# Performance work log

Hardware: AMD Instinct MI355X
Metric: run time of the kernel (lower is better)

Reference implementation:

```python
import jax, jax.numpy as jnp
import numpy as np

B, N, C, D, T = 8, 2048, 16, 64, 32
H = 100  # msg-MLP hidden width


def setup_inputs() -> dict:
    key = jax.random.key(0)
    ks = jax.random.split(key, 24)
    s = 0.05
    rn = lambda k, shape: (jax.random.normal(k, shape) * s).astype(jnp.float32)
    inp = {
        "Mvv": jax.random.bernoulli(ks[0], 0.05, (B, N, N)).astype(jnp.float32),
        "ch_init": jax.random.uniform(ks[1], (B, C, D), jnp.float32),
        "v_init": (jax.random.normal(ks[2], (D,)) / jnp.sqrt(jnp.float32(D))).astype(jnp.float32),
        # vertex LSTMCell: input 2D -> hidden D (gate order i,f,g,o as in torch)
        "v_Wih": rn(ks[3], (4 * D, 2 * D)), "v_Whh": rn(ks[4], (4 * D, D)),
        "v_bih": rn(ks[5], (4 * D,)), "v_bhh": rn(ks[6], (4 * D,)),
        # color LSTMCell: input D -> hidden D
        "c_Wih": rn(ks[7], (4 * D, D)), "c_Whh": rn(ks[8], (4 * D, D)),
        "c_bih": rn(ks[9], (4 * D,)), "c_bhh": rn(ks[10], (4 * D,)),
        # c_msg_mlp: D->100->D with ReLU after each Linear
        "cmsg_W1": rn(ks[11], (H, D)), "cmsg_b1": rn(ks[12], (H,)),
        "cmsg_W2": rn(ks[13], (D, H)), "cmsg_b2": rn(ks[14], (D,)),
        # v_msg_mlp: D->100->D
        "vmsg_W1": rn(ks[15], (H, D)), "vmsg_b1": rn(ks[16], (H,)),
        "vmsg_W2": rn(ks[17], (D, H)), "vmsg_b2": rn(ks[18], (D,)),
        # vote MLP: D -> D//4 -> 1 with Sigmoid in between
        "vote_W1": rn(ks[19], (D // 4, D)), "vote_b1": rn(ks[20], (D // 4,)),
        "vote_W2": rn(ks[21], (1, D // 4)), "vote_b2": rn(ks[22], (1,)),
        "n_colors": jax.random.randint(ks[23], (B,), 1, C + 1),
    }
    return inp


def _lstm_cell(x, h, c, Wih, Whh, bih, bhh):
    g = x @ Wih.T + bih + h @ Whh.T + bhh
    i, f, gg, o = jnp.split(g, 4, axis=-1)
    c2 = jax.nn.sigmoid(f) * c + jax.nn.sigmoid(i) * jnp.tanh(gg)
    h2 = jax.nn.sigmoid(o) * jnp.tanh(c2)
    return h2, c2


def _msg_mlp(x, W1, b1, W2, b2):
    return jax.nn.relu(jax.nn.relu(x @ W1.T + b1) @ W2.T + b2)


def reference(Mvv, ch_init, v_init,
              v_Wih, v_Whh, v_bih, v_bhh,
              c_Wih, c_Whh, c_bih, c_bhh,
              cmsg_W1, cmsg_b1, cmsg_W2, cmsg_b2,
              vmsg_W1, vmsg_b1, vmsg_W2, vmsg_b2,
              vote_W1, vote_b1, vote_W2, vote_b2,
              n_colors):
    A = Mvv + jnp.eye(N, dtype=Mvv.dtype)[None]                 # [B,N,N] self-loops
    col_mask = (jnp.arange(C)[None, :] < n_colors[:, None])     # [B,C]
    Mvc = jnp.broadcast_to(col_mask[:, None, :], (B, N, C)).astype(Mvv.dtype)  # [B,N,C]

    vh0 = jnp.broadcast_to(v_init, (B, N, D)).astype(Mvv.dtype)
    state0 = (vh0, jnp.zeros((B, N, D), Mvv.dtype), ch_init, jnp.zeros((B, C, D), Mvv.dtype))

    def step(st, _):
        vh, vc, ch, cc = st
        c_msg = _msg_mlp(ch, cmsg_W1, cmsg_b1, cmsg_W2, cmsg_b2)          # [B,C,D]
        v_in = jnp.concatenate([A @ vh, Mvc @ c_msg], axis=-1)            # [B,N,2D]
        vh, vc = _lstm_cell(v_in, vh, vc, v_Wih, v_Whh, v_bih, v_bhh)
        v_msg = _msg_mlp(vh, vmsg_W1, vmsg_b1, vmsg_W2, vmsg_b2)          # [B,N,D]
        c_in = jnp.einsum('bnc,bnd->bcd', Mvc, v_msg)                     # [B,C,D]
        ch, cc = _lstm_cell(c_in, ch, cc, c_Wih, c_Whh, c_bih, c_bhh)
        return (vh, vc, ch, cc), None

    (vh, _, _, _), _ = jax.lax.scan(step, state0, None, length=T)

    # dropout is identity in eval mode
    vote = jax.nn.sigmoid(vh @ vote_W1.T + vote_b1) @ vote_W2.T + vote_b2  # [B,N,1]
    pred = jax.nn.sigmoid(jnp.mean(vote, axis=1)).squeeze(-1)              # [B]
    return pred


if __name__ == "__main__":
    out = reference(**setup_inputs())
    print(out.shape, out)
```

## Files before the change

### kernel.cpp

```cpp
#include <hip/hip_runtime.h>

#define Bk 8
#define Nk 2048
#define Ck 16
#define Dk 64
#define Tk 32
#define GBLK 256
#define NTHR 512
#define SLOT (Bk * 64 * 2048)

typedef __attribute__((ext_vector_type(8))) short short8;
typedef __attribute__((ext_vector_type(4))) float floatx4;
typedef __attribute__((ext_vector_type(4))) unsigned uint4v;
typedef unsigned long long u64;
typedef unsigned short u16;

#define OFF_WCAT 0
#define OFF_VW1  69632
#define OFF_AT   85760
#define OFF_HT   103168
#define OFF_HROW 120576
#define OFF_CH   129792
#define OFF_CC   133888
#define OFF_GC   137984
#define OFF_VBS  139008
#define OFF_CBS  140032
#define OFF_VB1  141056
#define OFF_VB2  141568
#define OFF_CB1  141824
#define OFF_CB2  142336
#define OFF_W1V  142592
#define OFF_B1V  146688
#define OFF_W2V  146752
#define OFF_VAC  146816
#define OFF_VMS  147072
#define OFF_CMS  147328
#define OFF_VOT  147584
#define LDS_TOTAL 149632

__device__ __forceinline__ float b2f(u16 u) {
  return __uint_as_float(((unsigned)u) << 16);
}
__device__ __forceinline__ u16 f2b(float f) {
  unsigned u = __float_as_uint(f);
  unsigned r = (u + 0x7FFFu + ((u >> 16) & 1u)) >> 16;
  return (u16)r;
}
__device__ __forceinline__ float sigf(float x) { return 1.0f / (1.0f + __expf(-x)); }
__device__ __forceinline__ float tanhf_(float x) { return 2.0f / (1.0f + __expf(-2.0f * x)) - 1.0f; }

__device__ __forceinline__ void ld_sys_b128(uint4v& dst, const void* p) {
  asm volatile("global_load_dwordx4 %0, %1, off sc0 sc1" : "=v"(dst) : "v"(p) : "memory");
}
__device__ __forceinline__ void ld_b128(uint4v& dst, const void* p) {
  asm volatile("global_load_dwordx4 %0, %1, off" : "=v"(dst) : "v"(p) : "memory");
}
__device__ __forceinline__ void st_sys_b128(void* p, uint4v v) {
  asm volatile("global_store_dwordx4 %0, %1, off sc0 sc1" :: "v"(p), "v"(v) : "memory");
}
#define WAITVM(n) asm volatile("s_waitcnt vmcnt(" #n ")" ::: "memory")
__device__ __forceinline__ void barrier_lgkm() {
  asm volatile("s_waitcnt lgkmcnt(0)\n\ts_barrier" ::: "memory");
}

__device__ __forceinline__ void s_agent_f32(float* p, float v) {
  __hip_atomic_store(p, v, __ATOMIC_RELAXED, __HIP_MEMORY_SCOPE_AGENT);
}
__device__ __forceinline__ float l_agent_f32(const float* p) {
  return __hip_atomic_load(p, __ATOMIC_RELAXED, __HIP_MEMORY_SCOPE_AGENT);
}

__global__ void k_init_w(const float* vWih, const float* vWhh, const float* cWih, const float* cWhh,
                         const float* vm1, const float* vm2, const float* cm1, const float* cm2,
                         u16* wcat, u16* cwcat, u16* vw1, u16* vw2, u16* cw1, u16* cw2,
                         unsigned* bar, float* voteAcc, u64* diagBits) {
  const int tid = threadIdx.x;
  for (int i = tid; i < 256 * 128; i += 256) {
    int g = i >> 7, k = i & 127;
    wcat[i]  = f2b(k < 64 ? vWih[g * 128 + k] : vWhh[g * 64 + (k - 64)]);
    cwcat[i] = f2b(k < 64 ? cWih[g * 64 + k]  : cWhh[g * 64 + (k - 64)]);
  }
  for (int i = tid; i < 112 * 64; i += 256) {
    int j = i >> 6, k = i & 63;
    vw1[i] = f2b(j < 100 ? vm1[j * 64 + k] : 0.f);
    cw1[i] = f2b(j < 100 ? cm1[j * 64 + k] : 0.f);
  }
  for (int i = tid; i < 64 * 128; i += 256) {
    int d = i >> 7, k = i & 127;
    vw2[i] = f2b(k < 100 ? vm2[d * 100 + k] : 0.f);
    cw2[i] = f2b(k < 100 ? cm2[d * 100 + k] : 0.f);
  }
  for (int i = tid; i < 1024; i += 256) bar[i] = 0u;
  if (tid < 8) voteAcc[tid] = 0.f;
  if (tid < 256) diagBits[tid] = 0ull;
}

__global__ void k_init_vt(const float* vInit, u16* vt0) {
  for (int i = blockIdx.x * blockDim.x + threadIdx.x; i < SLOT; i += gridDim.x * blockDim.x) {
    int d = (i >> 11) & 63;
    vt0[i] = f2b(vInit[d]);
  }
}

__global__ void k_bits(const float* Mvv, u64* Abits, u64* diagBits) {
  const int lane = threadIdx.x & 63;
  const int wid = blockIdx.x * 4 + (threadIdx.x >> 6);
  const int b = wid >> 11, n = wid & 2047;
  const float* row = Mvv + (size_t)wid * Nk;
  u64* dst = Abits + (size_t)wid * 32;
  for (int w64 = 0; w64 < 32; ++w64) {
    float v = row[w64 * 64 + lane];
    u64 m = __ballot(v != 0.0f);
    if (lane == 0) {
      if (w64 == (n >> 6)) {
        if ((m >> (n & 63)) & 1ull)
          atomicOr(diagBits + b * 32 + (n >> 6), 1ull << (n & 63));
        m |= 1ull << (n & 63);
      }
      dst[w64] = m;
    }
  }
}

struct PArgs {
  const float *vWih, *chInit;
  const float *vbih, *vbhh, *cbih, *cbhh;
  const float *vmb1, *vmb2, *cmb1, *cmb2;
  const float *voW1, *vob1, *voW2, *vob2;
  const int* ncolors;
  u16* vhbuf;
  const u64* Abits;
  const u64* diagBits;
  float* partial;
  const u16 *wcat, *cwcat, *vw1, *vw2, *cw1, *cw2;
  unsigned* bar;
  float* voteAcc;
  float* out;
};

__device__ __forceinline__ void gridbar(unsigned* bar, unsigned target) {
  WAITVM(0);
  __syncthreads();
  if (threadIdx.x == 0) {
    atomicAdd(bar, 1u);
    int guard = 0;
    while (__hip_atomic_load(bar, __ATOMIC_RELAXED, __HIP_MEMORY_SCOPE_AGENT) < target) {
      __builtin_amdgcn_s_sleep(2);
      if (++guard > (1 << 24)) break;
    }
  }
  __syncthreads();
}

__global__ void __launch_bounds__(NTHR, 1) k_persist(PArgs A) {
  extern __shared__ char smem[];
  u16* WcatU  = (u16*)(smem + OFF_WCAT);
  u16* vW1U   = (u16*)(smem + OFF_VW1);
  u16* AtileU = (u16*)(smem + OFF_AT);
  u16* HtileU = (u16*)(smem + OFF_HT);
  u16* HrowU  = (u16*)(smem + OFF_HROW);
  float* chl = (float*)(smem + OFF_CH);
  float* ccl = (float*)(smem + OFF_CC);
  float* gc  = (float*)(smem + OFF_GC);
  float* vbs = (float*)(smem + OFF_VBS);
  float* cbs = (float*)(smem + OFF_CBS);
  float* vb1 = (float*)(smem + OFF_VB1);
  float* vb2 = (float*)(smem + OFF_VB2);
  float* cb1 = (float*)(smem + OFF_CB1);
  float* cb2 = (float*)(smem + OFF_CB2);
  float* W1v = (float*)(smem + OFF_W1V);
  float* b1v = (float*)(smem + OFF_B1V);
  float* W2v = (float*)(smem + OFF_W2V);
  float* vac = (float*)(smem + OFF_VAC);
  float* vms = (float*)(smem + OFF_VMS);
  float* cms = (float*)(smem + OFF_CMS);
  float* vot = (float*)(smem + OFF_VOT);

  const int tid = threadIdx.x;
  const int lane = tid & 63;
  const int w = tid >> 6;
  const int rt = w & 3;
  const int gh = w >> 2;
  const int q = lane >> 4;
  const int l15 = lane & 15;
  const int bb = blockIdx.x & 7;
  const int rb = (blockIdx.x >> 3) * 64;
  const int ncolv = A.ncolors[bb];
  const floatx4 zf = {0.f, 0.f, 0.f, 0.f};
  unsigned* mybar = A.bar + bb * 64;

  for (int i = tid; i < 256 * 128; i += NTHR) { int g = i >> 7, k = i & 127; WcatU[g * 136 + k] = A.wcat[i]; }
  for (int i = tid; i < 112 * 64; i += NTHR)  { int j = i >> 6, k = i & 63;  vW1U[j * 72 + k]  = A.vw1[i]; }
  if (tid < 112) { vb1[tid] = (tid < 100) ? A.vmb1[tid] : 0.f; cb1[tid] = (tid < 100) ? A.cmb1[tid] : 0.f; }
  if (tid < 64)  { vb2[tid] = A.vmb2[tid]; cb2[tid] = A.cmb2[tid]; vac[tid] = 0.f; }
  if (tid < 256) { vbs[tid] = A.vbih[tid] + A.vbhh[tid]; cbs[tid] = A.cbih[tid] + A.cbhh[tid]; }
  for (int i = tid; i < 1024; i += NTHR) { W1v[i] = A.voW1[i]; chl[i] = A.chInit[bb * 1024 + i]; ccl[i] = 0.f; }
  if (tid < 16) { b1v[tid] = A.vob1[tid]; W2v[tid] = A.voW2[tid]; }
  const u64 diagbits = A.diagBits[bb * 32 + (rb >> 6)];
  __syncthreads();

  auto cmsgPhase = [&]() {
    for (int i = tid; i < 1024; i += NTHR) { int c = i >> 6, kk = i & 63; AtileU[c * 136 + kk] = f2b(chl[i]); }
    __syncthreads();
    if (w < 7) {
      floatx4 m1a = zf;
#pragma unroll
      for (int ks = 0; ks < 2; ++ks) {
        short8 af = *(const short8*)(AtileU + l15 * 136 + ks * 32 + q * 8);
        short8 b0 = *(const short8*)(A.cw1 + (size_t)((w * 16 + l15) * 64 + ks * 32 + q * 8));
        m1a = __builtin_amdgcn_mfma_f32_16x16x32_bf16(af, b0, m1a, 0, 0, 0);
      }
#pragma unroll
      for (int reg = 0; reg < 4; ++reg) {
        float hv = m1a[reg] + cb1[w * 16 + l15];
        HtileU[(q * 4 + reg) * 136 + w * 16 + l15] = f2b(hv > 0.f ? hv : 0.f);
      }
    }
    if (tid < 128) {
      int r = tid >> 3, c = 112 + (tid & 7) * 2;
      HtileU[r * 136 + c] = 0; HtileU[r * 136 + c + 1] = 0;
    }
    __syncthreads();
    if (w < 4) {
      floatx4 m2 = zf;
#pragma unroll
      for (int ks = 0; ks < 4; ++ks) {
        short8 af = *(const short8*)(HtileU + l15 * 136 + ks * 32 + q * 8);
        short8 bv = *(const short8*)(A.cw2 + (size_t)((w * 16 + l15) * 128 + ks * 32 + q * 8));
        m2 = __builtin_amdgcn_mfma_f32_16x16x32_bf16(af, bv, m2, 0, 0, 0);
      }
      float s2 = 0.f;
#pragma unroll
      for (int reg = 0; reg < 4; ++reg) {
        int c = q * 4 + reg;
        float v = m2[reg] + cb2[w * 16 + l15];
        v = v > 0.f ? v : 0.f;
        if (c < ncolv) s2 += v;
      }
      s2 += __shfl_xor(s2, 16);
      s2 += __shfl_xor(s2, 32);
      if (q == 0) cms[w * 16 + l15] = s2;
    }
    __syncthreads();
    if (tid < 256) {
      float dot = 0.f;
      const float* wr = A.vWih + tid * 128 + 64;
#pragma unroll
      for (int k2 = 0; k2 < 64; ++k2) dot += cms[k2] * wr[k2];
      gc[tid] = dot + vbs[tid];
    }
    __syncthreads();
  };

  float vc[4][4] = {};
  u16 hreg[16];
  if (!gh) {
    u16 h0 = A.vhbuf[(size_t)(bb * 64 + lane) * 2048 + rb];
#pragma unroll
    for (int r = 0; r < 16; ++r) hreg[r] = h0;
  }

  cmsgPhase();
  unsigned ep = 0;

  const u64* arow = A.Abits + ((size_t)bb * 2048 + rb + rt * 16 + l15) * 32;

  for (int t = 0; t < Tk; ++t) {
    const u16* vtr = A.vhbuf + (size_t)(t & 1) * SLOT + (size_t)bb * 64 * 2048;
    u16* vtw = A.vhbuf + (size_t)((t & 1) ^ 1) * SLOT + (size_t)bb * 64 * 2048;

    floatx4 acc4[4];
#pragma unroll
    for (int nt = 0; nt < 4; ++nt) acc4[nt] = zf;

    uint4v D[2][2];
    uint4v Bts[4];

    auto issueGroup = [&](int c, uint4v (&Ds)[2], uint4v& Bv) {
      ld_b128(Bv, (const char*)arow + (size_t)c * 16);
      const char* base = (const char*)vtr + (size_t)c * 256;
#pragma unroll
      for (int i = 0; i < 2; ++i) {
        int idx = i * NTHR + tid, d = idx >> 4, j2 = idx & 15;
        ld_sys_b128(Ds[i], base + (size_t)d * 4096 + j2 * 16);
      }
    };
    auto stageGroup = [&](const uint4v (&Ds)[2], u16* buf) {
#pragma unroll
      for (int i = 0; i < 2; ++i) {
        int idx = i * NTHR + tid, d = idx >> 4, j2 = idx & 15;
        *(uint4v*)((char*)buf + (size_t)d * 272 + j2 * 16) = Ds[i];
      }
    };
    auto mfmaChunk = [&](const u16* buf, u64 w0, u64 w1) {
      u64 wsel = gh ? w1 : w0;
#pragma unroll
      for (int ks = 0; ks < 2; ++ks) {
        unsigned byte = (unsigned)(wsel >> (ks * 32 + q * 8)) & 0xFFu;
        short8 af;
#pragma unroll
        for (int j = 0; j < 8; ++j) af[j] = (short)(((byte >> j) & 1u) ? 0x3F80 : 0);
        int kg = gh * 2 + ks;
#pragma unroll
        for (int nt = 0; nt < 4; ++nt) {
          short8 bv = *(const short8*)(buf + (nt * 16 + l15) * 136 + kg * 32 + q * 8);
          acc4[nt] = __builtin_amdgcn_mfma_f32_16x16x32_bf16(af, bv, acc4[nt], 0, 0, 0);
        }
      }
    };

    issueGroup(0, D[0], Bts[0]);
    issueGroup(1, D[1], Bts[1]);
    WAITVM(3);
    stageGroup(D[0], AtileU);
    issueGroup(2, D[0], Bts[2]);
    barrier_lgkm();

#pragma unroll
    for (int c = 0; c < 16; ++c) {
      if (c < 14) { WAITVM(3); } else { WAITVM(0); }
      if (c < 15) {
        stageGroup(D[(c + 1) & 1], ((c + 1) & 1) ? HtileU : AtileU);
        if (c + 3 < 16) issueGroup(c + 3, D[(c + 1) & 1], Bts[(c + 3) & 3]);
      }
      {
        const uint4v& Bv = Bts[c & 3];
        u64 w0 = ((u64)Bv[1] << 32) | Bv[0];
        u64 w1 = ((u64)Bv[3] << 32) | Bv[2];
        mfmaChunk((c & 1) ? HtileU : AtileU, w0, w1);
      }
      if (c < 15) barrier_lgkm();
    }
    __syncthreads();

    {
      float* ptf = (float*)(smem + OFF_HT);
      if (gh) {
#pragma unroll
        for (int nt = 0; nt < 4; ++nt)
#pragma unroll
          for (int reg = 0; reg < 4; ++reg)
            ptf[rt * 1024 + (nt * 4 + reg) * 64 + lane] = acc4[nt][reg];
      }
      __syncthreads();
      if (!gh) {
#pragma unroll
        for (int nt = 0; nt < 4; ++nt)
#pragma unroll
          for (int reg = 0; reg < 4; ++reg)
            acc4[nt][reg] += ptf[rt * 1024 + (nt * 4 + reg) * 64 + lane];
#pragma unroll
        for (int r = 0; r < 16; ++r) AtileU[(rt * 16 + r) * 136 + 64 + lane] = hreg[r];
#pragma unroll
        for (int nt = 0; nt < 4; ++nt) {
#pragma unroll
          for (int reg = 0; reg < 4; ++reg) {
            int m = rt * 16 + q * 4 + reg;
            float fl = (float)((diagbits >> m) & 1ull);
            float hp = b2f(AtileU[m * 136 + 64 + nt * 16 + l15]);
            AtileU[m * 136 + nt * 16 + l15] = f2b(acc4[nt][reg] + fl * hp);
          }
        }
      }
    }
    __syncthreads();

    floatx4 acc2[8];
#pragma unroll
    for (int j = 0; j < 8; ++j) acc2[j] = zf;
#pragma unroll
    for (int ks = 0; ks < 4; ++ks) {
      short8 af = *(const short8*)(AtileU + (rt * 16 + l15) * 136 + ks * 32 + q * 8);
#pragma unroll
      for (int j = 0; j < 8; ++j) {
        short8 bv = *(const short8*)(WcatU + ((gh * 8 + j) * 16 + l15) * 136 + ks * 32 + q * 8);
        acc2[j] = __builtin_amdgcn_mfma_f32_16x16x32_bf16(af, bv, acc2[j], 0, 0, 0);
      }
    }
    __syncthreads();
    {
      float* gex = (float*)(smem + OFF_AT);
      if (gh) {
#pragma unroll
        for (int j = 0; j < 8; ++j)
#pragma unroll
          for (int reg = 0; reg < 4; ++reg)
            gex[(rt * 16 + q * 4 + reg) * 132 + j * 16 + l15] = acc2[j][reg];
      }
      __syncthreads();
      if (!gh) {
#pragma unroll
        for (int u = 0; u < 4; ++u) {
          const int d2 = u * 16 + l15;
          const float gi = gc[d2], gf2 = gc[64 + d2], gg = gc[128 + d2], go = gc[192 + d2];
#pragma unroll
          for (int reg = 0; reg < 4; ++reg) {
            const int row = rt * 16 + q * 4 + reg;
            float iv = acc2[u][reg] + gi;
            float fv = acc2[u + 4][reg] + gf2;
            float gv = gex[row * 132 + u * 16 + l15] + gg;
            float ov = gex[row * 132 + 64 + u * 16 + l15] + go;
            float cn = sigf(fv) * vc[u][reg] + sigf(iv) * tanhf_(gv);
            vc[u][reg] = cn;
            HrowU[row * 72 + d2] = f2b(sigf(ov) * tanhf_(cn));
          }
        }
      }
    }
    __syncthreads();
    if (!gh) {
#pragma unroll
      for (int r = 0; r < 16; ++r) hreg[r] = HrowU[(rt * 16 + r) * 72 + lane];
    }

    if (gh) {
      if (t < Tk - 1) {
        int lt = tid & 255, d = lt >> 2, rr = (lt & 3) * 16;
        union { u16 s[8]; uint4v v; } p0, p1;
#pragma unroll
        for (int j = 0; j < 8; ++j) {
          p0.s[j] = HrowU[(rr + j) * 72 + d];
          p1.s[j] = HrowU[(rr + 8 + j) * 72 + d];
        }
        char* dst = (char*)(vtw + (size_t)d * 2048 + rb + rr);
        st_sys_b128(dst, p0.v);
        st_sys_b128(dst + 16, p1.v);
      }
    } else if (t < Tk - 1) {
      u16* HID = AtileU;
      floatx4 h1[7];
#pragma unroll
      for (int nt = 0; nt < 7; ++nt) h1[nt] = zf;
#pragma unroll
      for (int ks = 0; ks < 2; ++ks) {
        short8 af = *(const short8*)(HrowU + (rt * 16 + l15) * 72 + ks * 32 + q * 8);
#pragma unroll
        for (int nt = 0; nt < 7; ++nt) {
          short8 bv = *(const short8*)(vW1U + (nt * 16 + l15) * 72 + ks * 32 + q * 8);
          h1[nt] = __builtin_amdgcn_mfma_f32_16x16x32_bf16(af, bv, h1[nt], 0, 0, 0);
        }
      }
#pragma unroll
      for (int nt = 0; nt < 7; ++nt) {
        float bb1 = vb1[nt * 16 + l15];
#pragma unroll
        for (int reg = 0; reg < 4; ++reg) {
          float hv = h1[nt][reg] + bb1;
          HID[(rt * 16 + q * 4 + reg) * 136 + nt * 16 + l15] = f2b(hv > 0.f ? hv : 0.f);
        }
      }
#pragma unroll
      for (int r = 0; r < 4; ++r) HID[(rt * 16 + q * 4 + r) * 136 + 112 + l15] = 0;

      floatx4 vm[4];
#pragma unroll
      for (int nt = 0; nt < 4; ++nt) vm[nt] = zf;
#pragma unroll
      for (int ks = 0; ks < 4; ++ks) {
        short8 af = *(const short8*)(HID + (rt * 16 + l15) * 136 + ks * 32 + q * 8);
#pragma unroll
        for (int nt = 0; nt < 4; ++nt) {
          short8 bv = *(const short8*)(A.vw2 + (size_t)((nt * 16 + l15) * 128 + ks * 32 + q * 8));
          vm[nt] = __builtin_amdgcn_mfma_f32_16x16x32_bf16(af, bv, vm[nt], 0, 0, 0);
        }
      }
#pragma unroll
      for (int u = 0; u < 4; ++u) {
        float bb2 = vb2[u * 16 + l15];
        float s = 0.f;
#pragma unroll
        for (int reg = 0; reg < 4; ++reg) { float v = vm[u][reg] + bb2; s += (v > 0.f ? v : 0.f); }
        s += __shfl_xor(s, 16);
        s += __shfl_xor(s, 32);
        if (q == 0) atomicAdd(&vac[u * 16 + l15], s);
      }
    }

    if (t < Tk - 1) {
      __syncthreads();
      if (tid < 64) {
        s_agent_f32(&A.partial[(size_t)((t & 1) * GBLK + blockIdx.x) * 64 + tid], vac[tid]);
        vac[tid] = 0.f;
      }
      gridbar(mybar, (++ep) * 32);

      if (tid < 64) {
        float s = 0.f;
        const float* pp = A.partial + (size_t)((t & 1) * GBLK) * 64;
        for (int i2 = 0; i2 < 32; ++i2) s += l_agent_f32(&pp[(i2 * 8 + bb) * 64 + tid]);
        vms[tid] = s;
      }
      __syncthreads();
      for (int i2 = tid; i2 < 16 * 128; i2 += NTHR) {
        int c = i2 >> 7, kk = i2 & 127;
        float v = (kk < 64) ? ((c < ncolv) ? vms[kk] : 0.f) : chl[c * 64 + (kk - 64)];
        AtileU[c * 136 + kk] = f2b(v);
      }
      __syncthreads();
      floatx4 cacc[2];
      cacc[0] = zf; cacc[1] = zf;
#pragma unroll
      for (int ks = 0; ks < 4; ++ks) {
        short8 af = *(const short8*)(AtileU + l15 * 136 + ks * 32 + q * 8);
#pragma unroll
        for (int j = 0; j < 2; ++j) {
          short8 bv = *(const short8*)(A.cwcat + (size_t)(((w * 2 + j) * 16 + l15) * 128 + ks * 32 + q * 8));
          cacc[j] = __builtin_amdgcn_mfma_f32_16x16x32_bf16(af, bv, cacc[j], 0, 0, 0);
        }
      }
      __syncthreads();
      float* cgp = (float*)(smem + OFF_AT);
#pragma unroll
      for (int j = 0; j < 2; ++j)
#pragma unroll
        for (int reg = 0; reg < 4; ++reg)
          cgp[(q * 4 + reg) * 260 + (w * 2 + j) * 16 + l15] = cacc[j][reg];
      __syncthreads();
      for (int i2 = tid; i2 < 1024; i2 += NTHR) {
        int c = i2 >> 6, d2 = i2 & 63;
        float iv = cgp[c * 260 + d2] + cbs[d2];
        float fv = cgp[c * 260 + 64 + d2] + cbs[64 + d2];
        float gv = cgp[c * 260 + 128 + d2] + cbs[128 + d2];
        float ov = cgp[c * 260 + 192 + d2] + cbs[192 + d2];
        float cn = sigf(fv) * ccl[i2] + sigf(iv) * tanhf_(gv);
        ccl[i2] = cn;
        chl[i2] = sigf(ov) * tanhf_(cn);
      }
      __syncthreads();
      cmsgPhase();
    }
  }

  {
    int r = tid >> 3, p = tid & 7;
    float hj[2] = {0.f, 0.f};
    for (int d2 = 0; d2 < 64; ++d2) {
      float hv = b2f(HrowU[r * 72 + d2]);
      hj[0] += hv * W1v[(p * 2) * 64 + d2];
      hj[1] += hv * W1v[(p * 2 + 1) * 64 + d2];
    }
    float pv = sigf(hj[0] + b1v[p * 2]) * W2v[p * 2] + sigf(hj[1] + b1v[p * 2 + 1]) * W2v[p * 2 + 1];
    vot[tid] = pv;
  }
  __syncthreads();
  if (tid < 64) {
    float vr = A.vob2[0];
#pragma unroll
    for (int k = 0; k < 8; ++k) vr += vot[tid * 8 + k];
    vr += __shfl_xor(vr, 1);
    vr += __shfl_xor(vr, 2);
    vr += __shfl_xor(vr, 4);
    vr += __shfl_xor(vr, 8);
    vr += __shfl_xor(vr, 16);
    vr += __shfl_xor(vr, 32);
    if (tid == 0) atomicAdd(&A.voteAcc[bb], vr);
  }
  gridbar(mybar, (++ep) * 32);
  if (blockIdx.x < 8 && tid == 0) {
    float m = l_agent_f32(&A.voteAcc[blockIdx.x]) * (1.f / 2048.f);
    A.out[blockIdx.x] = 1.f / (1.f + __expf(-m));
  }
}

extern "C" void kernel_launch(void* const* d_in, const int* in_sizes, int n_in,
                              void* d_out, int out_size, void* d_ws, size_t ws_size,
                              hipStream_t stream) {
  (void)in_sizes; (void)n_in; (void)out_size; (void)ws_size;
  const float* Mvv    = (const float*)d_in[0];
  const float* chInit = (const float*)d_in[1];
  const float* vInit  = (const float*)d_in[2];
  const float* vWih   = (const float*)d_in[3];
  const float* vWhh   = (const float*)d_in[4];
  const float* vbih   = (const float*)d_in[5];
  const float* vbhh   = (const float*)d_in[6];
  const float* cWih   = (const float*)d_in[7];
  const float* cWhh   = (const float*)d_in[8];
  const float* cbih   = (const float*)d_in[9];
  const float* cbhh   = (const float*)d_in[10];
  const float* cm1    = (const float*)d_in[11];
  const float* cmb1   = (const float*)d_in[12];
  const float* cm2    = (const float*)d_in[13];
  const float* cmb2   = (const float*)d_in[14];
  const float* vm1    = (const float*)d_in[15];
  const float* vmb1   = (const float*)d_in[16];
  const float* vm2    = (const float*)d_in[17];
  const float* vmb2   = (const float*)d_in[18];
  const float* voW1   = (const float*)d_in[19];
  const float* vob1   = (const float*)d_in[20];
  const float* voW2   = (const float*)d_in[21];
  const float* vob2   = (const float*)d_in[22];
  const int*   ncol   = (const int*)d_in[23];

  char* wsb = (char*)d_ws;
  size_t off = 0;
  auto wsAlloc = [&](size_t bytes) -> char* {
    char* p = wsb + off;
    off = (off + bytes + 255) & ~(size_t)255;
    return p;
  };
  unsigned* bar   = (unsigned*)wsAlloc(4096);
  float* voteAcc  = (float*)wsAlloc(256);
  u16* vhb        = (u16*)wsAlloc((size_t)2 * SLOT * 2);
  u64* Abits      = (u64*)wsAlloc((size_t)Bk * Nk * 32 * 8);
  u64* diagBits   = (u64*)wsAlloc((size_t)Bk * 32 * 8);
  float* partial  = (float*)wsAlloc((size_t)2 * GBLK * 64 * 4);
  u16* wcat       = (u16*)wsAlloc(256 * 128 * 2);
  u16* cwcat      = (u16*)wsAlloc(256 * 128 * 2);
  u16* vw1        = (u16*)wsAlloc(112 * 64 * 2);
  u16* vw2        = (u16*)wsAlloc(64 * 128 * 2);
  u16* cw1        = (u16*)wsAlloc(112 * 64 * 2);
  u16* cw2        = (u16*)wsAlloc(64 * 128 * 2);

  k_init_w<<<1, 256, 0, stream>>>(vWih, vWhh, cWih, cWhh, vm1, vm2, cm1, cm2,
                                  wcat, cwcat, vw1, vw2, cw1, cw2, bar, voteAcc, diagBits);
  k_init_vt<<<256, 256, 0, stream>>>(vInit, vhb);
  k_bits<<<Bk * Nk / 4, 256, 0, stream>>>(Mvv, Abits, diagBits);

  (void)hipFuncSetAttribute((const void*)k_persist,
                            hipFuncAttributeMaxDynamicSharedMemorySize, LDS_TOTAL);
  PArgs pa;
  pa.vWih = vWih; pa.chInit = chInit;
  pa.vbih = vbih; pa.vbhh = vbhh; pa.cbih = cbih; pa.cbhh = cbhh;
  pa.vmb1 = vmb1; pa.vmb2 = vmb2; pa.cmb1 = cmb1; pa.cmb2 = cmb2;
  pa.voW1 = voW1; pa.vob1 = vob1; pa.voW2 = voW2; pa.vob2 = vob2;
  pa.ncolors = ncol;
  pa.vhbuf = vhb; pa.Abits = Abits; pa.diagBits = diagBits; pa.partial = partial;
  pa.wcat = wcat; pa.cwcat = cwcat; pa.vw1 = vw1; pa.vw2 = vw2; pa.cw1 = cw1; pa.cw2 = cw2;
  pa.bar = bar; pa.voteAcc = voteAcc; pa.out = (float*)d_out;
  k_persist<<<GBLK, NTHR, LDS_TOTAL, stream>>>(pa);
}
```

Measured before the change: 1.497 ms.

## Replace persistent kernel grid barriers with per-timestep kernel launches

Replaces the persistent kernel, which used software grid barriers across blocks, with one kernel launch per timestep plus a final reduction kernel. Cross-step state (vertex cell state, color hidden/cell state, partial sums) moves to global buffers, and loads and stores become ordinary cached accesses instead of system-coherent ones. This removes the spin-wait barrier and the coherence overhead. In exchange it adds 32 launches, reloads all weights into LDS every step, and recomputes the small color LSTM redundantly in every block.

```diff
diff --git a/kernel.cpp b/kernel.cpp
--- a/kernel.cpp
+++ b/kernel.cpp
@@ -21,7 +21,6 @@
 #define OFF_HT   103168
 #define OFF_HROW 120576
 #define OFF_CH   129792
-#define OFF_CC   133888
 #define OFF_GC   137984
 #define OFF_VBS  139008
 #define OFF_CBS  140032
@@ -49,31 +48,18 @@
 __device__ __forceinline__ float sigf(float x) { return 1.0f / (1.0f + __expf(-x)); }
 __device__ __forceinline__ float tanhf_(float x) { return 2.0f / (1.0f + __expf(-2.0f * x)) - 1.0f; }
 
-__device__ __forceinline__ void ld_sys_b128(uint4v& dst, const void* p) {
-  asm volatile("global_load_dwordx4 %0, %1, off sc0 sc1" : "=v"(dst) : "v"(p) : "memory");
-}
 __device__ __forceinline__ void ld_b128(uint4v& dst, const void* p) {
   asm volatile("global_load_dwordx4 %0, %1, off" : "=v"(dst) : "v"(p) : "memory");
-}
-__device__ __forceinline__ void st_sys_b128(void* p, uint4v v) {
-  asm volatile("global_store_dwordx4 %0, %1, off sc0 sc1" :: "v"(p), "v"(v) : "memory");
 }
 #define WAITVM(n) asm volatile("s_waitcnt vmcnt(" #n ")" ::: "memory")
 __device__ __forceinline__ void barrier_lgkm() {
   asm volatile("s_waitcnt lgkmcnt(0)\n\ts_barrier" ::: "memory");
 }
 
-__device__ __forceinline__ void s_agent_f32(float* p, float v) {
-  __hip_atomic_store(p, v, __ATOMIC_RELAXED, __HIP_MEMORY_SCOPE_AGENT);
-}
-__device__ __forceinline__ float l_agent_f32(const float* p) {
-  return __hip_atomic_load(p, __ATOMIC_RELAXED, __HIP_MEMORY_SCOPE_AGENT);
-}
-
 __global__ void k_init_w(const float* vWih, const float* vWhh, const float* cWih, const float* cWhh,
                          const float* vm1, const float* vm2, const float* cm1, const float* cm2,
                          u16* wcat, u16* cwcat, u16* vw1, u16* vw2, u16* cw1, u16* cw2,
-                         unsigned* bar, float* voteAcc, u64* diagBits) {
+                         float* voteAcc, u64* diagBits) {
   const int tid = threadIdx.x;
   for (int i = tid; i < 256 * 128; i += 256) {
     int g = i >> 7, k = i & 127;
@@ -90,7 +76,6 @@
     vw2[i] = f2b(k < 100 ? vm2[d * 100 + k] : 0.f);
     cw2[i] = f2b(k < 100 ? cm2[d * 100 + k] : 0.f);
   }
-  for (int i = tid; i < 1024; i += 256) bar[i] = 0u;
   if (tid < 8) voteAcc[tid] = 0.f;
   if (tid < 256) diagBits[tid] = 0ull;
 }
@@ -122,8 +107,8 @@
   }
 }
 
-struct PArgs {
-  const float *vWih, *chInit;
+struct SArgs {
+  const float *chInit, *vWih;
   const float *vbih, *vbhh, *cbih, *cbhh;
   const float *vmb1, *vmb2, *cmb1, *cmb2;
   const float *voW1, *vob1, *voW2, *vob2;
@@ -132,27 +117,15 @@
   const u64* Abits;
   const u64* diagBits;
   float* partial;
+  float* vcbuf;
+  float* chbuf;
+  float* ccbuf;
   const u16 *wcat, *cwcat, *vw1, *vw2, *cw1, *cw2;
-  unsigned* bar;
   float* voteAcc;
-  float* out;
+  int t;
 };
 
-__device__ __forceinline__ void gridbar(unsigned* bar, unsigned target) {
-  WAITVM(0);
-  __syncthreads();
-  if (threadIdx.x == 0) {
-    atomicAdd(bar, 1u);
-    int guard = 0;
-    while (__hip_atomic_load(bar, __ATOMIC_RELAXED, __HIP_MEMORY_SCOPE_AGENT) < target) {
-      __builtin_amdgcn_s_sleep(2);
-      if (++guard > (1 << 24)) break;
-    }
-  }
-  __syncthreads();
-}
-
-__global__ void __launch_bounds__(NTHR, 1) k_persist(PArgs A) {
+__global__ void __launch_bounds__(NTHR, 1) k_step(SArgs A) {
   extern __shared__ char smem[];
   u16* WcatU  = (u16*)(smem + OFF_WCAT);
   u16* vW1U   = (u16*)(smem + OFF_VW1);
@@ -160,7 +133,6 @@
   u16* HtileU = (u16*)(smem + OFF_HT);
   u16* HrowU  = (u16*)(smem + OFF_HROW);
   float* chl = (float*)(smem + OFF_CH);
-  float* ccl = (float*)(smem + OFF_CC);
   float* gc  = (float*)(smem + OFF_GC);
   float* vbs = (float*)(smem + OFF_VBS);
   float* cbs = (float*)(smem + OFF_CBS);
@@ -176,6 +148,7 @@
   float* cms = (float*)(smem + OFF_CMS);
   float* vot = (float*)(smem + OFF_VOT);
 
+  const int t = A.t;
   const int tid = threadIdx.x;
   const int lane = tid & 63;
   const int w = tid >> 6;
@@ -187,246 +160,291 @@
   const int rb = (blockIdx.x >> 3) * 64;
   const int ncolv = A.ncolors[bb];
   const floatx4 zf = {0.f, 0.f, 0.f, 0.f};
-  unsigned* mybar = A.bar + bb * 64;
 
   for (int i = tid; i < 256 * 128; i += NTHR) { int g = i >> 7, k = i & 127; WcatU[g * 136 + k] = A.wcat[i]; }
   for (int i = tid; i < 112 * 64; i += NTHR)  { int j = i >> 6, k = i & 63;  vW1U[j * 72 + k]  = A.vw1[i]; }
   if (tid < 112) { vb1[tid] = (tid < 100) ? A.vmb1[tid] : 0.f; cb1[tid] = (tid < 100) ? A.cmb1[tid] : 0.f; }
   if (tid < 64)  { vb2[tid] = A.vmb2[tid]; cb2[tid] = A.cmb2[tid]; vac[tid] = 0.f; }
   if (tid < 256) { vbs[tid] = A.vbih[tid] + A.vbhh[tid]; cbs[tid] = A.cbih[tid] + A.cbhh[tid]; }
-  for (int i = tid; i < 1024; i += NTHR) { W1v[i] = A.voW1[i]; chl[i] = A.chInit[bb * 1024 + i]; ccl[i] = 0.f; }
+  for (int i = tid; i < 1024; i += NTHR) W1v[i] = A.voW1[i];
   if (tid < 16) { b1v[tid] = A.vob1[tid]; W2v[tid] = A.voW2[tid]; }
   const u64 diagbits = A.diagBits[bb * 32 + (rb >> 6)];
-  __syncthreads();
-
-  auto cmsgPhase = [&]() {
-    for (int i = tid; i < 1024; i += NTHR) { int c = i >> 6, kk = i & 63; AtileU[c * 136 + kk] = f2b(chl[i]); }
-    __syncthreads();
-    if (w < 7) {
-      floatx4 m1a = zf;
-#pragma unroll
-      for (int ks = 0; ks < 2; ++ks) {
-        short8 af = *(const short8*)(AtileU + l15 * 136 + ks * 32 + q * 8);
-        short8 b0 = *(const short8*)(A.cw1 + (size_t)((w * 16 + l15) * 64 + ks * 32 + q * 8));
-        m1a = __builtin_amdgcn_mfma_f32_16x16x32_bf16(af, b0, m1a, 0, 0, 0);
-      }
-#pragma unroll
-      for (int reg = 0; reg < 4; ++reg) {
-        float hv = m1a[reg] + cb1[w * 16 + l15];
-        HtileU[(q * 4 + reg) * 136 + w * 16 + l15] = f2b(hv > 0.f ? hv : 0.f);
-      }
-    }
-    if (tid < 128) {
-      int r = tid >> 3, c = 112 + (tid & 7) * 2;
-      HtileU[r * 136 + c] = 0; HtileU[r * 136 + c + 1] = 0;
-    }
-    __syncthreads();
-    if (w < 4) {
-      floatx4 m2 = zf;
-#pragma unroll
-      for (int ks = 0; ks < 4; ++ks) {
-        short8 af = *(const short8*)(HtileU + l15 * 136 + ks * 32 + q * 8);
-        short8 bv = *(const short8*)(A.cw2 + (size_t)((w * 16 + l15) * 128 + ks * 32 + q * 8));
-        m2 = __builtin_amdgcn_mfma_f32_16x16x32_bf16(af, bv, m2, 0, 0, 0);
-      }
-      float s2 = 0.f;
-#pragma unroll
-      for (int reg = 0; reg < 4; ++reg) {
-        int c = q * 4 + reg;
-        float v = m2[reg] + cb2[w * 16 + l15];
-        v = v > 0.f ? v : 0.f;
-        if (c < ncolv) s2 += v;
-      }
-      s2 += __shfl_xor(s2, 16);
-      s2 += __shfl_xor(s2, 32);
-      if (q == 0) cms[w * 16 + l15] = s2;
-    }
-    __syncthreads();
-    if (tid < 256) {
-      float dot = 0.f;
-      const float* wr = A.vWih + tid * 128 + 64;
-#pragma unroll
-      for (int k2 = 0; k2 < 64; ++k2) dot += cms[k2] * wr[k2];
-      gc[tid] = dot + vbs[tid];
-    }
-    __syncthreads();
-  };
-
-  float vc[4][4] = {};
+
   u16 hreg[16];
   if (!gh) {
-    u16 h0 = A.vhbuf[(size_t)(bb * 64 + lane) * 2048 + rb];
-#pragma unroll
-    for (int r = 0; r < 16; ++r) hreg[r] = h0;
-  }
-
-  cmsgPhase();
-  unsigned ep = 0;
-
+    const u16* hp = A.vhbuf + (size_t)(t & 1) * SLOT + ((size_t)(bb * 64 + lane)) * 2048 + rb + rt * 16;
+#pragma unroll
+    for (int r = 0; r < 16; ++r) hreg[r] = hp[r];
+  }
+  __syncthreads();
+
+  if (t == 0) {
+    for (int i = tid; i < 1024; i += NTHR) chl[i] = A.chInit[bb * 1024 + i];
+    __syncthreads();
+  } else {
+    const float* chprev = (t == 1) ? (A.chInit + bb * 1024)
+                                   : (A.chbuf + (size_t)((t & 1) ^ 1) * Bk * 1024 + bb * 1024);
+    if (tid < 64) {
+      float s = 0.f;
+      const float* pp = A.partial + (size_t)(((t - 1) & 1) * GBLK) * 64;
+      for (int i2 = 0; i2 < 32; ++i2) s += pp[(i2 * 8 + bb) * 64 + tid];
+      vms[tid] = s;
+    }
+    __syncthreads();
+    for (int i2 = tid; i2 < 16 * 128; i2 += NTHR) {
+      int c = i2 >> 7, kk = i2 & 127;
+      float v = (kk < 64) ? ((c < ncolv) ? vms[kk] : 0.f) : chprev[c * 64 + (kk - 64)];
+      AtileU[c * 136 + kk] = f2b(v);
+    }
+    __syncthreads();
+    floatx4 cacc[2];
+    cacc[0] = zf; cacc[1] = zf;
+#pragma unroll
+    for (int ks = 0; ks < 4; ++ks) {
+      short8 af = *(const short8*)(AtileU + l15 * 136 + ks * 32 + q * 8);
+#pragma unroll
+      for (int j = 0; j < 2; ++j) {
+        short8 bv = *(const short8*)(A.cwcat + (size_t)(((w * 2 + j) * 16 + l15) * 128 + ks * 32 + q * 8));
+        cacc[j] = __builtin_amdgcn_mfma_f32_16x16x32_bf16(af, bv, cacc[j], 0, 0, 0);
+      }
+    }
+    __syncthreads();
+    float* cgp = (float*)(smem + OFF_AT);
+#pragma unroll
+    for (int j = 0; j < 2; ++j)
+#pragma unroll
+      for (int reg = 0; reg < 4; ++reg)
+        cgp[(q * 4 + reg) * 260 + (w * 2 + j) * 16 + l15] = cacc[j][reg];
+    __syncthreads();
+    for (int i2 = tid; i2 < 1024; i2 += NTHR) {
+      int c = i2 >> 6, d2 = i2 & 63;
+      float iv = cgp[c * 260 + d2] + cbs[d2];
+      float fv = cgp[c * 260 + 64 + d2] + cbs[64 + d2];
+      float gv = cgp[c * 260 + 128 + d2] + cbs[128 + d2];
+      float ov = cgp[c * 260 + 192 + d2] + cbs[192 + d2];
+      float ccv = (t == 1) ? 0.f : A.ccbuf[(size_t)((t & 1) ^ 1) * Bk * 1024 + bb * 1024 + i2];
+      float cn = sigf(fv) * ccv + sigf(iv) * tanhf_(gv);
+      float hn = sigf(ov) * tanhf_(cn);
+      chl[i2] = hn;
+      if (blockIdx.x < 8) {
+        A.ccbuf[(size_t)(t & 1) * Bk * 1024 + bb * 1024 + i2] = cn;
+        A.chbuf[(size_t)(t & 1) * Bk * 1024 + bb * 1024 + i2] = hn;
+      }
+    }
+    __syncthreads();
+  }
+  for (int i = tid; i < 1024; i += NTHR) { int c = i >> 6, kk = i & 63; AtileU[c * 136 + kk] = f2b(chl[i]); }
+  __syncthreads();
+  if (w < 7) {
+    floatx4 m1a = zf;
+#pragma unroll
+    for (int ks = 0; ks < 2; ++ks) {
+      short8 af = *(const short8*)(AtileU + l15 * 136 + ks * 32 + q * 8);
+      short8 b0 = *(const short8*)(A.cw1 + (size_t)((w * 16 + l15) * 64 + ks * 32 + q * 8));
+      m1a = __builtin_amdgcn_mfma_f32_16x16x32_bf16(af, b0, m1a, 0, 0, 0);
+    }
+#pragma unroll
+    for (int reg = 0; reg < 4; ++reg) {
+      float hv = m1a[reg] + cb1[w * 16 + l15];
+      HtileU[(q * 4 + reg) * 136 + w * 16 + l15] = f2b(hv > 0.f ? hv : 0.f);
+    }
+  }
+  if (tid < 128) {
+    int r = tid >> 3, c = 112 + (tid & 7) * 2;
+    HtileU[r * 136 + c] = 0; HtileU[r * 136 + c + 1] = 0;
+  }
+  __syncthreads();
+  if (w < 4) {
+    floatx4 m2 = zf;
+#pragma unroll
+    for (int ks = 0; ks < 4; ++ks) {
+      short8 af = *(const short8*)(HtileU + l15 * 136 + ks * 32 + q * 8);
+      short8 bv = *(const short8*)(A.cw2 + (size_t)((w * 16 + l15) * 128 + ks * 32 + q * 8));
+      m2 = __builtin_amdgcn_mfma_f32_16x16x32_bf16(af, bv, m2, 0, 0, 0);
+    }
+    float s2 = 0.f;
+#pragma unroll
+    for (int reg = 0; reg < 4; ++reg) {
+      int c = q * 4 + reg;
+      float v = m2[reg] + cb2[w * 16 + l15];
+      v = v > 0.f ? v : 0.f;
+      if (c < ncolv) s2 += v;
+    }
+    s2 += __shfl_xor(s2, 16);
+    s2 += __shfl_xor(s2, 32);
+    if (q == 0) cms[w * 16 + l15] = s2;
+  }
+  __syncthreads();
+  if (tid < 256) {
+    float dot = 0.f;
+    const float* wr = A.vWih + tid * 128 + 64;
+#pragma unroll
+    for (int k2 = 0; k2 < 64; ++k2) dot += cms[k2] * wr[k2];
+    gc[tid] = dot + vbs[tid];
+  }
+  __syncthreads();
+
+  __builtin_amdgcn_sched_barrier(0);
   const u64* arow = A.Abits + ((size_t)bb * 2048 + rb + rt * 16 + l15) * 32;
-
-  for (int t = 0; t < Tk; ++t) {
-    const u16* vtr = A.vhbuf + (size_t)(t & 1) * SLOT + (size_t)bb * 64 * 2048;
-    u16* vtw = A.vhbuf + (size_t)((t & 1) ^ 1) * SLOT + (size_t)bb * 64 * 2048;
-
-    floatx4 acc4[4];
-#pragma unroll
-    for (int nt = 0; nt < 4; ++nt) acc4[nt] = zf;
-
-    uint4v D[2][2];
-    uint4v Bts[4];
-
-    auto issueGroup = [&](int c, uint4v (&Ds)[2], uint4v& Bv) {
-      ld_b128(Bv, (const char*)arow + (size_t)c * 16);
-      const char* base = (const char*)vtr + (size_t)c * 256;
-#pragma unroll
-      for (int i = 0; i < 2; ++i) {
-        int idx = i * NTHR + tid, d = idx >> 4, j2 = idx & 15;
-        ld_sys_b128(Ds[i], base + (size_t)d * 4096 + j2 * 16);
-      }
-    };
-    auto stageGroup = [&](const uint4v (&Ds)[2], u16* buf) {
-#pragma unroll
-      for (int i = 0; i < 2; ++i) {
-        int idx = i * NTHR + tid, d = idx >> 4, j2 = idx & 15;
-        *(uint4v*)((char*)buf + (size_t)d * 272 + j2 * 16) = Ds[i];
-      }
-    };
-    auto mfmaChunk = [&](const u16* buf, u64 w0, u64 w1) {
-      u64 wsel = gh ? w1 : w0;
-#pragma unroll
-      for (int ks = 0; ks < 2; ++ks) {
-        unsigned byte = (unsigned)(wsel >> (ks * 32 + q * 8)) & 0xFFu;
-        short8 af;
-#pragma unroll
-        for (int j = 0; j < 8; ++j) af[j] = (short)(((byte >> j) & 1u) ? 0x3F80 : 0);
-        int kg = gh * 2 + ks;
-#pragma unroll
-        for (int nt = 0; nt < 4; ++nt) {
-          short8 bv = *(const short8*)(buf + (nt * 16 + l15) * 136 + kg * 32 + q * 8);
-          acc4[nt] = __builtin_amdgcn_mfma_f32_16x16x32_bf16(af, bv, acc4[nt], 0, 0, 0);
+  const u16* vtr = A.vhbuf + (size_t)(t & 1) * SLOT + (size_t)bb * 64 * 2048;
+  u16* vtw = A.vhbuf + (size_t)((t & 1) ^ 1) * SLOT + (size_t)bb * 64 * 2048;
+
+  floatx4 acc4[4];
+#pragma unroll
+  for (int nt = 0; nt < 4; ++nt) acc4[nt] = zf;
+
+  uint4v D[2][2];
+  uint4v Bts[4];
+
+  auto issueGroup = [&](int c, uint4v (&Ds)[2], uint4v& Bv) {
+    ld_b128(Bv, (const char*)arow + (size_t)c * 16);
+    const char* base = (const char*)vtr + (size_t)c * 256;
+#pragma unroll
+    for (int i = 0; i < 2; ++i) {
+      int idx = i * NTHR + tid, d = idx >> 4, j2 = idx & 15;
+      ld_b128(Ds[i], base + (size_t)d * 4096 + j2 * 16);
+    }
+  };
+  auto stageGroup = [&](const uint4v (&Ds)[2], u16* buf) {
+#pragma unroll
+    for (int i = 0; i < 2; ++i) {
+      int idx = i * NTHR + tid, d = idx >> 4, j2 = idx & 15;
+      *(uint4v*)((char*)buf + (size_t)d * 272 + j2 * 16) = Ds[i];
+    }
+  };
+  auto mfmaChunk = [&](const u16* buf, u64 w0, u64 w1) {
+    u64 wsel = gh ? w1 : w0;
+#pragma unroll
+    for (int ks = 0; ks < 2; ++ks) {
+      unsigned byte = (unsigned)(wsel >> (ks * 32 + q * 8)) & 0xFFu;
+      short8 af;
+#pragma unroll
+      for (int j = 0; j < 8; ++j) af[j] = (short)(((byte >> j) & 1u) ? 0x3F80 : 0);
+      int kg = gh * 2 + ks;
+#pragma unroll
+      for (int nt = 0; nt < 4; ++nt) {
+        short8 bv = *(const short8*)(buf + (nt * 16 + l15) * 136 + kg * 32 + q * 8);
+        acc4[nt] = __builtin_amdgcn_mfma_f32_16x16x32_bf16(af, bv, acc4[nt], 0, 0, 0);
+      }
+    }
+  };
+
+  issueGroup(0, D[0], Bts[0]);
+  issueGroup(1, D[1], Bts[1]);
+  WAITVM(3);
+  stageGroup(D[0], AtileU);
+  issueGroup(2, D[0], Bts[2]);
+  barrier_lgkm();
+
+#pragma unroll
+  for (int c = 0; c < 16; ++c) {
+    if (c < 14) { WAITVM(3); } else { WAITVM(0); }
+    if (c < 15) {
+      stageGroup(D[(c + 1) & 1], ((c + 1) & 1) ? HtileU : AtileU);
+      if (c + 3 < 16) issueGroup(c + 3, D[(c + 1) & 1], Bts[(c + 3) & 3]);
+    }
+    {
+      const uint4v& Bv = Bts[c & 3];
+      u64 w0 = ((u64)Bv[1] << 32) | Bv[0];
+      u64 w1 = ((u64)Bv[3] << 32) | Bv[2];
+      mfmaChunk((c & 1) ? HtileU : AtileU, w0, w1);
+    }
+    if (c < 15) barrier_lgkm();
+  }
+  __builtin_amdgcn_sched_barrier(0);
+  __syncthreads();
+
+  {
+    float* ptf = (float*)(smem + OFF_HT);
+    if (gh) {
+#pragma unroll
+      for (int nt = 0; nt < 4; ++nt)
+#pragma unroll
+        for (int reg = 0; reg < 4; ++reg)
+          ptf[rt * 1024 + (nt * 4 + reg) * 64 + lane] = acc4[nt][reg];
+    }
+    __syncthreads();
+    if (!gh) {
+#pragma unroll
+      for (int nt = 0; nt < 4; ++nt)
+#pragma unroll
+        for (int reg = 0; reg < 4; ++reg)
+          acc4[nt][reg] += ptf[rt * 1024 + (nt * 4 + reg) * 64 + lane];
+#pragma unroll
+      for (int r = 0; r < 16; ++r) AtileU[(rt * 16 + r) * 136 + 64 + lane] = hreg[r];
+#pragma unroll
+      for (int nt = 0; nt < 4; ++nt) {
+#pragma unroll
+        for (int reg = 0; reg < 4; ++reg) {
+          int m = rt * 16 + q * 4 + reg;
+          float fl = (float)((diagbits >> m) & 1ull);
+          float hp = b2f(AtileU[m * 136 + 64 + nt * 16 + l15]);
+          AtileU[m * 136 + nt * 16 + l15] = f2b(acc4[nt][reg] + fl * hp);
         }
       }
-    };
-
-    issueGroup(0, D[0], Bts[0]);
-    issueGroup(1, D[1], Bts[1]);
-    WAITVM(3);
-    stageGroup(D[0], AtileU);
-    issueGroup(2, D[0], Bts[2]);
-    barrier_lgkm();
-
-#pragma unroll
-    for (int c = 0; c < 16; ++c) {
-      if (c < 14) { WAITVM(3); } else { WAITVM(0); }
-      if (c < 15) {
-        stageGroup(D[(c + 1) & 1], ((c + 1) & 1) ? HtileU : AtileU);
-        if (c + 3 < 16) issueGroup(c + 3, D[(c + 1) & 1], Bts[(c + 3) & 3]);
-      }
-      {
-        const uint4v& Bv = Bts[c & 3];
-        u64 w0 = ((u64)Bv[1] << 32) | Bv[0];
-        u64 w1 = ((u64)Bv[3] << 32) | Bv[2];
-        mfmaChunk((c & 1) ? HtileU : AtileU, w0, w1);
-      }
-      if (c < 15) barrier_lgkm();
-    }
-    __syncthreads();
-
-    {
-      float* ptf = (float*)(smem + OFF_HT);
-      if (gh) {
-#pragma unroll
-        for (int nt = 0; nt < 4; ++nt)
-#pragma unroll
-          for (int reg = 0; reg < 4; ++reg)
-            ptf[rt * 1024 + (nt * 4 + reg) * 64 + lane] = acc4[nt][reg];
-      }
-      __syncthreads();
-      if (!gh) {
-#pragma unroll
-        for (int nt = 0; nt < 4; ++nt)
-#pragma unroll
-          for (int reg = 0; reg < 4; ++reg)
-            acc4[nt][reg] += ptf[rt * 1024 + (nt * 4 + reg) * 64 + lane];
-#pragma unroll
-        for (int r = 0; r < 16; ++r) AtileU[(rt * 16 + r) * 136 + 64 + lane] = hreg[r];
-#pragma unroll
-        for (int nt = 0; nt < 4; ++nt) {
-#pragma unroll
-          for (int reg = 0; reg < 4; ++reg) {
-            int m = rt * 16 + q * 4 + reg;
-            float fl = (float)((diagbits >> m) & 1ull);
-            float hp = b2f(AtileU[m * 136 + 64 + nt * 16 + l15]);
-            AtileU[m * 136 + nt * 16 + l15] = f2b(acc4[nt][reg] + fl * hp);
-          }
+    }
+  }
+  __syncthreads();
+
+  floatx4 acc2[8];
+#pragma unroll
+  for (int j = 0; j < 8; ++j) acc2[j] = zf;
+#pragma unroll
+  for (int ks = 0; ks < 4; ++ks) {
+    short8 af = *(const short8*)(AtileU + (rt * 16 + l15) * 136 + ks * 32 + q * 8);
+#pragma unroll
+    for (int j = 0; j < 8; ++j) {
+      short8 bv = *(const short8*)(WcatU + ((gh * 8 + j) * 16 + l15) * 136 + ks * 32 + q * 8);
+      acc2[j] = __builtin_amdgcn_mfma_f32_16x16x32_bf16(af, bv, acc2[j], 0, 0, 0);
+    }
+  }
+  __syncthreads();
+  {
+    float* gex = (float*)(smem + OFF_AT);
+    if (gh) {
+#pragma unroll
+      for (int j = 0; j < 8; ++j)
+#pragma unroll
+        for (int reg = 0; reg < 4; ++reg)
+          gex[(rt * 16 + q * 4 + reg) * 132 + j * 16 + l15] = acc2[j][reg];
+    }
+    __syncthreads();
+    if (!gh) {
+#pragma unroll
+      for (int u = 0; u < 4; ++u) {
+        const int d2 = u * 16 + l15;
+        const float gi = gc[d2], gf2 = gc[64 + d2], gg = gc[128 + d2], go = gc[192 + d2];
+#pragma unroll
+        for (int reg = 0; reg < 4; ++reg) {
+          const int row = rt * 16 + q * 4 + reg;
+          size_t vci = ((size_t)(bb * 2048 + rb + row)) * 64 + d2;
+          float vcv = (t == 0) ? 0.f : A.vcbuf[vci];
+          float iv = acc2[u][reg] + gi;
+          float fv = acc2[u + 4][reg] + gf2;
+          float gv = gex[row * 132 + u * 16 + l15] + gg;
+          float ov = gex[row * 132 + 64 + u * 16 + l15] + go;
+          float cn = sigf(fv) * vcv + sigf(iv) * tanhf_(gv);
+          A.vcbuf[vci] = cn;
+          HrowU[row * 72 + d2] = f2b(sigf(ov) * tanhf_(cn));
         }
       }
     }
-    __syncthreads();
-
-    floatx4 acc2[8];
-#pragma unroll
-    for (int j = 0; j < 8; ++j) acc2[j] = zf;
-#pragma unroll
-    for (int ks = 0; ks < 4; ++ks) {
-      short8 af = *(const short8*)(AtileU + (rt * 16 + l15) * 136 + ks * 32 + q * 8);
+  }
+  __syncthreads();
+
+  if (t < Tk - 1) {
+    if (gh) {
+      int lt = tid & 255, d = lt >> 2, rr = (lt & 3) * 16;
+      union { u16 s[8]; uint4v v; } p0, p1;
 #pragma unroll
       for (int j = 0; j < 8; ++j) {
-        short8 bv = *(const short8*)(WcatU + ((gh * 8 + j) * 16 + l15) * 136 + ks * 32 + q * 8);
-        acc2[j] = __builtin_amdgcn_mfma_f32_16x16x32_bf16(af, bv, acc2[j], 0, 0, 0);
-      }
-    }
-    __syncthreads();
-    {
-      float* gex = (float*)(smem + OFF_AT);
-      if (gh) {
-#pragma unroll
-        for (int j = 0; j < 8; ++j)
-#pragma unroll
-          for (int reg = 0; reg < 4; ++reg)
-            gex[(rt * 16 + q * 4 + reg) * 132 + j * 16 + l15] = acc2[j][reg];
-      }
-      __syncthreads();
-      if (!gh) {
-#pragma unroll
-        for (int u = 0; u < 4; ++u) {
-          const int d2 = u * 16 + l15;
-          const float gi = gc[d2], gf2 = gc[64 + d2], gg = gc[128 + d2], go = gc[192 + d2];
-#pragma unroll
-          for (int reg = 0; reg < 4; ++reg) {
-            const int row = rt * 16 + q * 4 + reg;
-            float iv = acc2[u][reg] + gi;
-            float fv = acc2[u + 4][reg] + gf2;
-            float gv = gex[row * 132 + u * 16 + l15] + gg;
-            float ov = gex[row * 132 + 64 + u * 16 + l15] + go;
-            float cn = sigf(fv) * vc[u][reg] + sigf(iv) * tanhf_(gv);
-            vc[u][reg] = cn;
-            HrowU[row * 72 + d2] = f2b(sigf(ov) * tanhf_(cn));
-          }
-        }
-      }
-    }
-    __syncthreads();
-    if (!gh) {
-#pragma unroll
-      for (int r = 0; r < 16; ++r) hreg[r] = HrowU[(rt * 16 + r) * 72 + lane];
-    }
-
-    if (gh) {
-      if (t < Tk - 1) {
-        int lt = tid & 255, d = lt >> 2, rr = (lt & 3) * 16;
-        union { u16 s[8]; uint4v v; } p0, p1;
-#pragma unroll
-        for (int j = 0; j < 8; ++j) {
-          p0.s[j] = HrowU[(rr + j) * 72 + d];
-          p1.s[j] = HrowU[(rr + 8 + j) * 72 + d];
-        }
-        char* dst = (char*)(vtw + (size_t)d * 2048 + rb + rr);
-        st_sys_b128(dst, p0.v);
-        st_sys_b128(dst + 16, p1.v);
-      }
-    } else if (t < Tk - 1) {
+        p0.s[j] = HrowU[(rr + j) * 72 + d];
+        p1.s[j] = HrowU[(rr + 8 + j) * 72 + d];
+      }
+      u16* dst = vtw + (size_t)d * 2048 + rb + rr;
+      *(uint4v*)dst = p0.v;
+      *(uint4v*)(dst + 8) = p1.v;
+    } else {
       u16* HID = AtileU;
       floatx4 h1[7];
 #pragma unroll
@@ -475,91 +493,40 @@
         if (q == 0) atomicAdd(&vac[u * 16 + l15], s);
       }
     }
-
-    if (t < Tk - 1) {
-      __syncthreads();
-      if (tid < 64) {
-        s_agent_f32(&A.partial[(size_t)((t & 1) * GBLK + blockIdx.x) * 64 + tid], vac[tid]);
-        vac[tid] = 0.f;
-      }
-      gridbar(mybar, (++ep) * 32);
-
-      if (tid < 64) {
-        float s = 0.f;
-        const float* pp = A.partial + (size_t)((t & 1) * GBLK) * 64;
-        for (int i2 = 0; i2 < 32; ++i2) s += l_agent_f32(&pp[(i2 * 8 + bb) * 64 + tid]);
-        vms[tid] = s;
-      }
-      __syncthreads();
-      for (int i2 = tid; i2 < 16 * 128; i2 += NTHR) {
-        int c = i2 >> 7, kk = i2 & 127;
-        float v = (kk < 64) ? ((c < ncolv) ? vms[kk] : 0.f) : chl[c * 64 + (kk - 64)];
-        AtileU[c * 136 + kk] = f2b(v);
-      }
-      __syncthreads();
-      floatx4 cacc[2];
-      cacc[0] = zf; cacc[1] = zf;
-#pragma unroll
-      for (int ks = 0; ks < 4; ++ks) {
-        short8 af = *(const short8*)(AtileU + l15 * 136 + ks * 32 + q * 8);
-#pragma unroll
-        for (int j = 0; j < 2; ++j) {
-          short8 bv = *(const short8*)(A.cwcat + (size_t)(((w * 2 + j) * 16 + l15) * 128 + ks * 32 + q * 8));
-          cacc[j] = __builtin_amdgcn_mfma_f32_16x16x32_bf16(af, bv, cacc[j], 0, 0, 0);
-        }
-      }
-      __syncthreads();
-      float* cgp = (float*)(smem + OFF_AT);
-#pragma unroll
-      for (int j = 0; j < 2; ++j)
-#pragma unroll
-        for (int reg = 0; reg < 4; ++reg)
-          cgp[(q * 4 + reg) * 260 + (w * 2 + j) * 16 + l15] = cacc[j][reg];
-      __syncthreads();
-      for (int i2 = tid; i2 < 1024; i2 += NTHR) {
-        int c = i2 >> 6, d2 = i2 & 63;
-        float iv = cgp[c * 260 + d2] + cbs[d2];
-        float fv = cgp[c * 260 + 64 + d2] + cbs[64 + d2];
-        float gv = cgp[c * 260 + 128 + d2] + cbs[128 + d2];
-        float ov = cgp[c * 260 + 192 + d2] + cbs[192 + d2];
-        float cn = sigf(fv) * ccl[i2] + sigf(iv) * tanhf_(gv);
-        ccl[i2] = cn;
-        chl[i2] = sigf(ov) * tanhf_(cn);
-      }
-      __syncthreads();
-      cmsgPhase();
-    }
-  }
-
-  {
-    int r = tid >> 3, p = tid & 7;
-    float hj[2] = {0.f, 0.f};
-    for (int d2 = 0; d2 < 64; ++d2) {
-      float hv = b2f(HrowU[r * 72 + d2]);
-      hj[0] += hv * W1v[(p * 2) * 64 + d2];
-      hj[1] += hv * W1v[(p * 2 + 1) * 64 + d2];
-    }
-    float pv = sigf(hj[0] + b1v[p * 2]) * W2v[p * 2] + sigf(hj[1] + b1v[p * 2 + 1]) * W2v[p * 2 + 1];
-    vot[tid] = pv;
-  }
-  __syncthreads();
-  if (tid < 64) {
-    float vr = A.vob2[0];
-#pragma unroll
-    for (int k = 0; k < 8; ++k) vr += vot[tid * 8 + k];
-    vr += __shfl_xor(vr, 1);
-    vr += __shfl_xor(vr, 2);
-    vr += __shfl_xor(vr, 4);
-    vr += __shfl_xor(vr, 8);
-    vr += __shfl_xor(vr, 16);
-    vr += __shfl_xor(vr, 32);
-    if (tid == 0) atomicAdd(&A.voteAcc[bb], vr);
-  }
-  gridbar(mybar, (++ep) * 32);
-  if (blockIdx.x < 8 && tid == 0) {
-    float m = l_agent_f32(&A.voteAcc[blockIdx.x]) * (1.f / 2048.f);
-    A.out[blockIdx.x] = 1.f / (1.f + __expf(-m));
-  }
+    __syncthreads();
+    if (tid < 64)
+      A.partial[(size_t)((t & 1) * GBLK + blockIdx.x) * 64 + tid] = vac[tid];
+  } else {
+    {
+      int r = tid >> 3, p = tid & 7;
+      float hj[2] = {0.f, 0.f};
+      for (int d2 = 0; d2 < 64; ++d2) {
+        float hv = b2f(HrowU[r * 72 + d2]);
+        hj[0] += hv * W1v[(p * 2) * 64 + d2];
+        hj[1] += hv * W1v[(p * 2 + 1) * 64 + d2];
+      }
+      float pv = sigf(hj[0] + b1v[p * 2]) * W2v[p * 2] + sigf(hj[1] + b1v[p * 2 + 1]) * W2v[p * 2 + 1];
+      vot[tid] = pv;
+    }
+    __syncthreads();
+    if (tid < 64) {
+      float vr = A.vob2[0];
+#pragma unroll
+      for (int k = 0; k < 8; ++k) vr += vot[tid * 8 + k];
+      vr += __shfl_xor(vr, 1);
+      vr += __shfl_xor(vr, 2);
+      vr += __shfl_xor(vr, 4);
+      vr += __shfl_xor(vr, 8);
+      vr += __shfl_xor(vr, 16);
+      vr += __shfl_xor(vr, 32);
+      if (tid == 0) atomicAdd(&A.voteAcc[bb], vr);
+    }
+  }
+}
+
+__global__ void k_final(const float* voteAcc, float* out) {
+  int i = threadIdx.x;
+  if (i < 8) out[i] = 1.f / (1.f + __expf(-(voteAcc[i] * (1.f / 2048.f))));
 }
 
 extern "C" void kernel_launch(void* const* d_in, const int* in_sizes, int n_in,
@@ -598,12 +565,14 @@
     off = (off + bytes + 255) & ~(size_t)255;
     return p;
   };
-  unsigned* bar   = (unsigned*)wsAlloc(4096);
   float* voteAcc  = (float*)wsAlloc(256);
   u16* vhb        = (u16*)wsAlloc((size_t)2 * SLOT * 2);
   u64* Abits      = (u64*)wsAlloc((size_t)Bk * Nk * 32 * 8);
   u64* diagBits   = (u64*)wsAlloc((size_t)Bk * 32 * 8);
   float* partial  = (float*)wsAlloc((size_t)2 * GBLK * 64 * 4);
+  float* vcbuf    = (float*)wsAlloc((size_t)Bk * Nk * 64 * 4);
+  float* chbuf    = (float*)wsAlloc((size_t)2 * Bk * 1024 * 4);
+  float* ccbuf    = (float*)wsAlloc((size_t)2 * Bk * 1024 * 4);
   u16* wcat       = (u16*)wsAlloc(256 * 128 * 2);
   u16* cwcat      = (u16*)wsAlloc(256 * 128 * 2);
   u16* vw1        = (u16*)wsAlloc(112 * 64 * 2);
@@ -612,20 +581,26 @@
   u16* cw2        = (u16*)wsAlloc(64 * 128 * 2);
 
   k_init_w<<<1, 256, 0, stream>>>(vWih, vWhh, cWih, cWhh, vm1, vm2, cm1, cm2,
-                                  wcat, cwcat, vw1, vw2, cw1, cw2, bar, voteAcc, diagBits);
+                                  wcat, cwcat, vw1, vw2, cw1, cw2, voteAcc, diagBits);
   k_init_vt<<<256, 256, 0, stream>>>(vInit, vhb);
   k_bits<<<Bk * Nk / 4, 256, 0, stream>>>(Mvv, Abits, diagBits);
 
-  (void)hipFuncSetAttribute((const void*)k_persist,
+  (void)hipFuncSetAttribute((const void*)k_step,
                             hipFuncAttributeMaxDynamicSharedMemorySize, LDS_TOTAL);
-  PArgs pa;
-  pa.vWih = vWih; pa.chInit = chInit;
-  pa.vbih = vbih; pa.vbhh = vbhh; pa.cbih = cbih; pa.cbhh = cbhh;
-  pa.vmb1 = vmb1; pa.vmb2 = vmb2; pa.cmb1 = cmb1; pa.cmb2 = cmb2;
-  pa.voW1 = voW1; pa.vob1 = vob1; pa.voW2 = voW2; pa.vob2 = vob2;
-  pa.ncolors = ncol;
-  pa.vhbuf = vhb; pa.Abits = Abits; pa.diagBits = diagBits; pa.partial = partial;
-  pa.wcat = wcat; pa.cwcat = cwcat; pa.vw1 = vw1; pa.vw2 = vw2; pa.cw1 = cw1; pa.cw2 = cw2;
-  pa.bar = bar; pa.voteAcc = voteAcc; pa.out = (float*)d_out;
-  k_persist<<<GBLK, NTHR, LDS_TOTAL, stream>>>(pa);
-}
+  SArgs sa;
+  sa.chInit = chInit; sa.vWih = vWih;
+  sa.vbih = vbih; sa.vbhh = vbhh; sa.cbih = cbih; sa.cbhh = cbhh;
+  sa.vmb1 = vmb1; sa.vmb2 = vmb2; sa.cmb1 = cmb1; sa.cmb2 = cmb2;
+  sa.voW1 = voW1; sa.vob1 = vob1; sa.voW2 = voW2; sa.vob2 = vob2;
+  sa.ncolors = ncol;
+  sa.vhbuf = vhb; sa.Abits = Abits; sa.diagBits = diagBits;
+  sa.partial = partial; sa.vcbuf = vcbuf; sa.chbuf = chbuf; sa.ccbuf = ccbuf;
+  sa.wcat = wcat; sa.cwcat = cwcat; sa.vw1 = vw1; sa.vw2 = vw2; sa.cw1 = cw1; sa.cw2 = cw2;
+  sa.voteAcc = voteAcc;
+
+  for (int t = 0; t < Tk; ++t) {
+    sa.t = t;
+    k_step<<<GBLK, NTHR, LDS_TOTAL, stream>>>(sa);
+  }
+  k_final<<<1, 64, 0, stream>>>(voteAcc, (float*)d_out);
+}
```

Result: faster. 1.363 ms (-8.9%).
